# Performance work log

Measured on AMD Instinct MI355X. Metric: run time of the kernel, lower is better.

## Reference

```python
import jax, jax.numpy as jnp
import numpy as np

E = 200_000   # edges (messages)
T = 2_000_000 # triplets
N = 20_000    # atoms/nodes
H = 128       # hidden_channels
INT = 64      # int_emb_size
BAS = 8       # basis_emb_size
OUT_EMB = 256 # out_emb_channels
NRAD = 6
SBF_DIM = 7 * 6  # num_spherical * num_radial = 42
NB = 4        # num_blocks
OUTC = 1      # num_targets


def setup_inputs() -> dict:
    key = jax.random.key(0)
    ks = iter(jax.random.split(key, 64))

    def w(shape):
        # glorot-ish scaled weights, stored as [in, out] for x @ W
        return jax.random.normal(next(ks), shape, jnp.float32) / np.sqrt(shape[-2])

    return dict(
        x=jax.random.normal(next(ks), (E, H), jnp.float32),
        rbf=jax.random.normal(next(ks), (E, NRAD), jnp.float32),
        sbf=jax.random.normal(next(ks), (T, SBF_DIM), jnp.float32),
        # interaction block params, stacked over NB blocks
        W_rbf1=w((NB, NRAD, BAS)), W_rbf2=w((NB, BAS, H)),
        W_sbf1=w((NB, SBF_DIM, BAS)), W_sbf2=w((NB, BAS, INT)),
        W_kj=w((NB, H, H)), b_kj=jnp.zeros((NB, H), jnp.float32),
        W_ji=w((NB, H, H)), b_ji=jnp.zeros((NB, H), jnp.float32),
        W_down=w((NB, H, INT)), W_up=w((NB, INT, H)),
        Wb=w((NB, 2, H, H)), bb=jnp.zeros((NB, 2, H), jnp.float32),   # num_before_skip=1 -> 2 linears
        Wa=w((NB, 4, H, H)), ba=jnp.zeros((NB, 4, H), jnp.float32),   # num_after_skip=2 -> 4 linears
        W_lin=w((NB, H, H)), b_lin=jnp.zeros((NB, H), jnp.float32),
        # output block params, stacked over NB+1 blocks
        Wo_rbf=w((NB + 1, NRAD, H)),
        Wo_up=w((NB + 1, H, OUT_EMB)), bo_up=jnp.zeros((NB + 1, OUT_EMB), jnp.float32),
        Wo_lins=w((NB + 1, 3, OUT_EMB, OUT_EMB)), bo_lins=jnp.zeros((NB + 1, 3, OUT_EMB), jnp.float32),
        Wo_out=w((NB + 1, OUT_EMB, OUTC)),
        idx_kj=jax.random.randint(next(ks), (T,), 0, E, jnp.int32),
        idx_ji=jax.random.randint(next(ks), (T,), 0, E, jnp.int32),
        idx_i=jax.random.randint(next(ks), (E,), 0, N, jnp.int32),
        num_nodes=N,
    )


def _interaction(b, x, rbf, sbf, idx_kj, idx_ji, p):
    act = jax.nn.silu
    x_ji = act(x @ p['W_ji'][b] + p['b_ji'][b])
    x_kj = act(x @ p['W_kj'][b] + p['b_kj'][b])
    rbf_t = (rbf @ p['W_rbf1'][b]) @ p['W_rbf2'][b]          # [E,H]
    x_kj = act((x_kj * rbf_t) @ p['W_down'][b])              # [E,INT]
    sbf_t = (sbf @ p['W_sbf1'][b]) @ p['W_sbf2'][b]          # [T,INT]
    m = x_kj[idx_kj] * sbf_t                                  # triplet gather [T,INT]
    agg = jax.ops.segment_sum(m, idx_ji, num_segments=x.shape[0])  # scatter-add [E,INT]
    x_kj = act(agg @ p['W_up'][b])                            # [E,H]
    h = x_ji + x_kj
    # residual layers before skip (1 layer = 2 linears)
    h = h + act(act(h @ p['Wb'][b, 0] + p['bb'][b, 0]) @ p['Wb'][b, 1] + p['bb'][b, 1])
    h = act(h @ p['W_lin'][b] + p['b_lin'][b]) + x
    # residual layers after skip (2 layers = 4 linears)
    for l in range(2):
        h = h + act(act(h @ p['Wa'][b, 2 * l] + p['ba'][b, 2 * l]) @ p['Wa'][b, 2 * l + 1] + p['ba'][b, 2 * l + 1])
    return h


def _output(b, x, rbf, idx_i, num_nodes, p):
    act = jax.nn.silu
    t = (rbf @ p['Wo_rbf'][b]) * x                            # [E,H]
    t = jax.ops.segment_sum(t, idx_i, num_segments=num_nodes) # [N,H]
    t = t @ p['Wo_up'][b] + p['bo_up'][b]
    for l in range(3):
        t = act(t @ p['Wo_lins'][b, l] + p['bo_lins'][b, l])
    return t @ p['Wo_out'][b]                                 # [N,OUTC]


def reference(x, rbf, sbf, W_rbf1, W_rbf2, W_sbf1, W_sbf2, W_kj, b_kj, W_ji, b_ji,
              W_down, W_up, Wb, bb, Wa, ba, W_lin, b_lin,
              Wo_rbf, Wo_up, bo_up, Wo_lins, bo_lins, Wo_out,
              idx_kj, idx_ji, idx_i, num_nodes):
    p = dict(W_rbf1=W_rbf1, W_rbf2=W_rbf2, W_sbf1=W_sbf1, W_sbf2=W_sbf2,
             W_kj=W_kj, b_kj=b_kj, W_ji=W_ji, b_ji=b_ji, W_down=W_down, W_up=W_up,
             Wb=Wb, bb=bb, Wa=Wa, ba=ba, W_lin=W_lin, b_lin=b_lin,
             Wo_rbf=Wo_rbf, Wo_up=Wo_up, bo_up=bo_up,
             Wo_lins=Wo_lins, bo_lins=bo_lins, Wo_out=Wo_out)
    P = _output(0, x, rbf, idx_i, num_nodes, p)
    for b in range(NB):  # fixed small layer loop
        x = _interaction(b, x, rbf, sbf, idx_kj, idx_ji, p)
        P = P + _output(b + 1, x, rbf, idx_i, num_nodes, p)
    return P
```

## Files before the change

kernel.cpp:

```cpp
#include <hip/hip_runtime.h>
#include <hip/hip_bf16.h>

#define E_EDGES 200000
#define T_TRIP  2000000
#define N_NODES 20000
#define H_DIM   128
#define INT_DIM 64
#define BAS     8
#define OUT_EMB 256
#define NRAD    6
#define SBF_D   42
#define NB      4

typedef __attribute__((ext_vector_type(8))) __bf16 bf16x8;
typedef __attribute__((ext_vector_type(4))) float f32x4;
typedef unsigned short u16;

__device__ __forceinline__ float silu_f(float v) { return v / (1.0f + __expf(-v)); }

__device__ __forceinline__ u16 f2bf(float f) {
    unsigned int u = __float_as_uint(f);
    u += 0x7FFF + ((u >> 16) & 1);
    return (u16)(u >> 16);
}
__device__ __forceinline__ float bf2f(u16 h) {
    return __uint_as_float(((unsigned int)h) << 16);
}

__device__ __forceinline__ void st_split4(char* H, char* L, int row, int col0, int stride,
                                          const float v[4]) {
    ushort4 hh, ll;
    u16 h0 = f2bf(v[0]); ll.x = f2bf(v[0] - bf2f(h0)); hh.x = h0;
    u16 h1 = f2bf(v[1]); ll.y = f2bf(v[1] - bf2f(h1)); hh.y = h1;
    u16 h2 = f2bf(v[2]); ll.z = f2bf(v[2] - bf2f(h2)); hh.z = h2;
    u16 h3 = f2bf(v[3]); ll.w = f2bf(v[3] - bf2f(h3)); hh.w = h3;
    int off = (row * stride + col0 * 2) ^ ((row & 7) << 4);
    *reinterpret_cast<ushort4*>(H + off) = hh;
    *reinterpret_cast<ushort4*>(L + off) = ll;
}
__device__ __forceinline__ void ld_split4(const char* H, const char* L, int row, int col0,
                                          int stride, float v[4]) {
    int off = (row * stride + col0 * 2) ^ ((row & 7) << 4);
    ushort4 hh = *reinterpret_cast<const ushort4*>(H + off);
    ushort4 ll = *reinterpret_cast<const ushort4*>(L + off);
    v[0] = bf2f(hh.x) + bf2f(ll.x);
    v[1] = bf2f(hh.y) + bf2f(ll.y);
    v[2] = bf2f(hh.z) + bf2f(ll.z);
    v[3] = bf2f(hh.w) + bf2f(ll.w);
}

struct BF8x4 { bf16x8 h[4]; bf16x8 l[4]; };

__device__ __forceinline__ BF8x4 loadB128f(const u16* __restrict__ Bh, const u16* __restrict__ Bl,
                                           int k0, int wn, int l15, int khalf)
{
    BF8x4 f;
    #pragma unroll
    for (int n = 0; n < 4; ++n) {
        size_t bo = (size_t)(wn * 64 + n * 16 + l15) * 128 + k0 + khalf;
        f.h[n] = *reinterpret_cast<const bf16x8*>(Bh + bo);
        f.l[n] = *reinterpret_cast<const bf16x8*>(Bl + bo);
    }
    return f;
}
__device__ __forceinline__ BF8x4 loadB64f(const u16* __restrict__ Bh, const u16* __restrict__ Bl,
                                          int k0, int wn, int l15, int khalf)
{
    BF8x4 f;
    #pragma unroll
    for (int n = 0; n < 4; ++n) {
        size_t bo = (size_t)(wn * 64 + n * 16 + l15) * 64 + k0 + khalf;
        f.h[n] = *reinterpret_cast<const bf16x8*>(Bh + bo);
        f.l[n] = *reinterpret_cast<const bf16x8*>(Bl + bo);
    }
    return f;
}
__device__ __forceinline__ BF8x4 loadB256f(const u16* __restrict__ Bh, const u16* __restrict__ Bl,
                                           int k0, int wn, int l15, int khalf)
{
    BF8x4 f;
    #pragma unroll
    for (int n = 0; n < 4; ++n) {
        size_t bo = (size_t)(wn * 64 + n * 16 + l15) * 256 + k0 + khalf;
        f.h[n] = *reinterpret_cast<const bf16x8*>(Bh + bo);
        f.l[n] = *reinterpret_cast<const bf16x8*>(Bl + bo);
    }
    return f;
}

__device__ __forceinline__ void mfma_cluster(
    const char* AH, const char* AL, int k0, int wm, int l15, int khalf,
    const BF8x4& b, f32x4 acc[2][4])
{
    __builtin_amdgcn_s_setprio(1);
    #pragma unroll
    for (int m = 0; m < 2; ++m) {
        int row = wm * 32 + m * 16 + l15;
        int off = (row * 256 + (k0 + khalf) * 2) ^ ((row & 7) << 4);
        bf16x8 ah = *reinterpret_cast<const bf16x8*>(AH + off);
        bf16x8 al = *reinterpret_cast<const bf16x8*>(AL + off);
        #pragma unroll
        for (int n = 0; n < 4; ++n) {
            acc[m][n] = __builtin_amdgcn_mfma_f32_16x16x32_bf16(b.h[n], ah, acc[m][n], 0, 0, 0);
            acc[m][n] = __builtin_amdgcn_mfma_f32_16x16x32_bf16(b.h[n], al, acc[m][n], 0, 0, 0);
            acc[m][n] = __builtin_amdgcn_mfma_f32_16x16x32_bf16(b.l[n], ah, acc[m][n], 0, 0, 0);
        }
    }
    __builtin_amdgcn_s_setprio(0);
}
__device__ __forceinline__ void mfma_cluster64(
    const char* AH, const char* AL, int k0, int wm, int l15, int khalf,
    const BF8x4& b, f32x4 acc[2][4])
{
    __builtin_amdgcn_s_setprio(1);
    #pragma unroll
    for (int m = 0; m < 2; ++m) {
        int row = wm * 32 + m * 16 + l15;
        int off = (row * 128 + (k0 + khalf) * 2) ^ ((row & 7) << 4);
        bf16x8 ah = *reinterpret_cast<const bf16x8*>(AH + off);
        bf16x8 al = *reinterpret_cast<const bf16x8*>(AL + off);
        #pragma unroll
        for (int n = 0; n < 4; ++n) {
            acc[m][n] = __builtin_amdgcn_mfma_f32_16x16x32_bf16(b.h[n], ah, acc[m][n], 0, 0, 0);
            acc[m][n] = __builtin_amdgcn_mfma_f32_16x16x32_bf16(b.h[n], al, acc[m][n], 0, 0, 0);
            acc[m][n] = __builtin_amdgcn_mfma_f32_16x16x32_bf16(b.l[n], ah, acc[m][n], 0, 0, 0);
        }
    }
    __builtin_amdgcn_s_setprio(0);
}
__device__ __forceinline__ void mfma_cluster512(
    const char* AH, const char* AL, int k0, int l15, int khalf,
    const BF8x4& b, f32x4 acc[2][4])
{
    __builtin_amdgcn_s_setprio(1);
    #pragma unroll
    for (int m = 0; m < 2; ++m) {
        int row = m * 16 + l15;
        int off = (row * 512 + (k0 + khalf) * 2) ^ ((row & 7) << 4);
        bf16x8 ah = *reinterpret_cast<const bf16x8*>(AH + off);
        bf16x8 al = *reinterpret_cast<const bf16x8*>(AL + off);
        #pragma unroll
        for (int n = 0; n < 4; ++n) {
            acc[m][n] = __builtin_amdgcn_mfma_f32_16x16x32_bf16(b.h[n], ah, acc[m][n], 0, 0, 0);
            acc[m][n] = __builtin_amdgcn_mfma_f32_16x16x32_bf16(b.h[n], al, acc[m][n], 0, 0, 0);
            acc[m][n] = __builtin_amdgcn_mfma_f32_16x16x32_bf16(b.l[n], ah, acc[m][n], 0, 0, 0);
        }
    }
    __builtin_amdgcn_s_setprio(0);
}

__device__ __forceinline__ void mm128_pipe(
    const char* AH, const char* AL,
    const u16* __restrict__ Bh, const u16* __restrict__ Bl, BF8x4& pre,
    const u16* __restrict__ nBh, const u16* __restrict__ nBl,
    int wm, int wn, int l15, int khalf, f32x4 acc[2][4])
{
    BF8x4 c0 = pre;
    BF8x4 c1 = loadB128f(Bh, Bl, 32, wn, l15, khalf);
    mfma_cluster(AH, AL, 0, wm, l15, khalf, c0, acc);
    BF8x4 c2 = loadB128f(Bh, Bl, 64, wn, l15, khalf);
    mfma_cluster(AH, AL, 32, wm, l15, khalf, c1, acc);
    BF8x4 c3 = loadB128f(Bh, Bl, 96, wn, l15, khalf);
    mfma_cluster(AH, AL, 64, wm, l15, khalf, c2, acc);
    if (nBh) pre = loadB128f(nBh, nBl, 0, wn, l15, khalf);
    mfma_cluster(AH, AL, 96, wm, l15, khalf, c3, acc);
}
__device__ __forceinline__ void mm64_pipe(
    const char* AH, const char* AL,
    const u16* __restrict__ Bh, const u16* __restrict__ Bl, BF8x4& pre,
    const u16* __restrict__ nBh, const u16* __restrict__ nBl,
    int wm, int wn, int l15, int khalf, f32x4 acc[2][4])
{
    BF8x4 c0 = pre;
    BF8x4 c1 = loadB64f(Bh, Bl, 32, wn, l15, khalf);
    mfma_cluster64(AH, AL, 0, wm, l15, khalf, c0, acc);
    if (nBh) pre = loadB128f(nBh, nBl, 0, wn, l15, khalf);
    mfma_cluster64(AH, AL, 32, wm, l15, khalf, c1, acc);
}

__global__ __launch_bounds__(256) void wprep(
    const float* __restrict__ src, u16* __restrict__ hi,
    u16* __restrict__ lo, int K, int N)
{
    int e = blockIdx.x * 256 + threadIdx.x;
    int total = K * N;
    if (e >= total) return;
    size_t base = (size_t)blockIdx.y * total;
    float a = src[base + e];
    int k = e / N, n = e - k * N;
    u16 h = f2bf(a);
    u16 l = f2bf(a - bf2f(h));
    hi[base + (size_t)n * K + k] = h;
    lo[base + (size_t)n * K + k] = l;
}

__global__ __launch_bounds__(256, 2) void pre_fuse(
    const float* __restrict__ X, const float* __restrict__ rbf,
    const float* __restrict__ W1,
    const u16* __restrict__ Wjih, const u16* __restrict__ Wjil, const float* __restrict__ bji,
    const u16* __restrict__ Wkjh, const u16* __restrict__ Wkjl, const float* __restrict__ bkj,
    const float* __restrict__ Wr2,
    const u16* __restrict__ Wdnh, const u16* __restrict__ Wdnl,
    float* __restrict__ E1, float* __restrict__ C1)
{
    __shared__ u16 XH[64 * 128], XL[64 * 128];
    __shared__ u16 IH[64 * 128], IL[64 * 128];

    const int tid  = threadIdx.x;
    const int lane = tid & 63;
    const int w    = tid >> 6;
    const int wm   = w >> 1, wn = w & 1;
    const int bm   = blockIdx.x * 64;
    const int l15  = lane & 15;
    const int khalf = (lane >> 4) * 8;
    const int r4   = (lane >> 4) * 4;

    BF8x4 pre = loadB128f(Wjih, Wjil, 0, wn, l15, khalf);

    {
        int r  = tid >> 2;
        int c0 = (tid & 3) * 32;
        const float* p = &X[(size_t)(bm + r) * H_DIM + c0];
        const int swz = (r & 7) << 4;
        #pragma unroll
        for (int q = 0; q < 8; ++q) {
            float4 f = *reinterpret_cast<const float4*>(p + q * 4);
            float vv[4] = {f.x, f.y, f.z, f.w};
            u16 h[4], l[4];
            #pragma unroll
            for (int j = 0; j < 4; ++j) {
                h[j] = f2bf(vv[j]);
                l[j] = f2bf(vv[j] - bf2f(h[j]));
            }
            int off = (r * 256 + c0 * 2 + q * 8) ^ swz;
            *reinterpret_cast<ushort4*>((char*)XH + off) = make_ushort4(h[0], h[1], h[2], h[3]);
            *reinterpret_cast<ushort4*>((char*)XL + off) = make_ushort4(l[0], l[1], l[2], l[3]);
        }
    }
    __syncthreads();

    {
        f32x4 acc[2][4] = {};
        mm128_pipe((char*)XH, (char*)XL, Wjih, Wjil, pre, Wkjh, Wkjl,
                   wm, wn, l15, khalf, acc);
        #pragma unroll
        for (int n = 0; n < 4; ++n) {
            int col0 = wn * 64 + n * 16 + r4;
            float4 bv = *reinterpret_cast<const float4*>(&bji[col0]);
            #pragma unroll
            for (int m = 0; m < 2; ++m) {
                int row = wm * 32 + m * 16 + l15;
                float4 o;
                o.x = silu_f(acc[m][n][0] + bv.x);
                o.y = silu_f(acc[m][n][1] + bv.y);
                o.z = silu_f(acc[m][n][2] + bv.z);
                o.w = silu_f(acc[m][n][3] + bv.w);
                *reinterpret_cast<float4*>(&E1[(size_t)(bm + row) * H_DIM + col0]) = o;
            }
        }
    }
    {
        f32x4 acc[2][4] = {};
        mm128_pipe((char*)XH, (char*)XL, Wkjh, Wkjl, pre, nullptr, nullptr,
                   wm, wn, l15, khalf, acc);
        float r8v[2][8];
        #pragma unroll
        for (int m = 0; m < 2; ++m) {
            int grow = bm + wm * 32 + m * 16 + l15;
            const float2* rp = reinterpret_cast<const float2*>(&rbf[(size_t)grow * NRAD]);
            float2 q0 = rp[0], q1 = rp[1], q2 = rp[2];
            float rv[NRAD] = {q0.x, q0.y, q1.x, q1.y, q2.x, q2.y};
            #pragma unroll
            for (int j = 0; j < 8; ++j) r8v[m][j] = 0.f;
            #pragma unroll
            for (int k = 0; k < NRAD; ++k)
                #pragma unroll
                for (int j = 0; j < 8; ++j)
                    r8v[m][j] = fmaf(rv[k], W1[k * BAS + j], r8v[m][j]);
        }
        #pragma unroll
        for (int n = 0; n < 4; ++n) {
            int col0 = wn * 64 + n * 16 + r4;
            float4 bvf = *reinterpret_cast<const float4*>(&bkj[col0]);
            float bv[4] = {bvf.x, bvf.y, bvf.z, bvf.w};
            float wrv[8][4];
            #pragma unroll
            for (int j = 0; j < 8; ++j) {
                float4 wf = *reinterpret_cast<const float4*>(&Wr2[j * H_DIM + col0]);
                wrv[j][0] = wf.x; wrv[j][1] = wf.y; wrv[j][2] = wf.z; wrv[j][3] = wf.w;
            }
            #pragma unroll
            for (int m = 0; m < 2; ++m) {
                int row = wm * 32 + m * 16 + l15;
                float v[4];
                #pragma unroll
                for (int r = 0; r < 4; ++r) {
                    float t = silu_f(acc[m][n][r] + bv[r]);
                    float g = 0.f;
                    #pragma unroll
                    for (int j = 0; j < 8; ++j)
                        g = fmaf(r8v[m][j], wrv[j][r], g);
                    v[r] = t * g;
                }
                st_split4((char*)IH, (char*)IL, row, col0, 256, v);
            }
        }
    }
    __syncthreads();

    {
        f32x4 acc[2][2] = {};
        #pragma unroll
        for (int k0 = 0; k0 < 128; k0 += 32) {
            bf16x8 bh[2], bl[2];
            #pragma unroll
            for (int n = 0; n < 2; ++n) {
                size_t bo = (size_t)(wn * 32 + n * 16 + l15) * 128 + k0 + khalf;
                bh[n] = *reinterpret_cast<const bf16x8*>(Wdnh + bo);
                bl[n] = *reinterpret_cast<const bf16x8*>(Wdnl + bo);
            }
            __builtin_amdgcn_s_setprio(1);
            #pragma unroll
            for (int m = 0; m < 2; ++m) {
                int row = wm * 32 + m * 16 + l15;
                int off = (row * 256 + (k0 + khalf) * 2) ^ ((row & 7) << 4);
                bf16x8 ah = *reinterpret_cast<const bf16x8*>((const char*)IH + off);
                bf16x8 al = *reinterpret_cast<const bf16x8*>((const char*)IL + off);
                #pragma unroll
                for (int n = 0; n < 2; ++n) {
                    acc[m][n] = __builtin_amdgcn_mfma_f32_16x16x32_bf16(bh[n], ah, acc[m][n], 0, 0, 0);
                    acc[m][n] = __builtin_amdgcn_mfma_f32_16x16x32_bf16(bh[n], al, acc[m][n], 0, 0, 0);
                    acc[m][n] = __builtin_amdgcn_mfma_f32_16x16x32_bf16(bl[n], ah, acc[m][n], 0, 0, 0);
                }
            }
            __builtin_amdgcn_s_setprio(0);
        }
        #pragma unroll
        for (int n = 0; n < 2; ++n) {
            int col0 = wn * 32 + n * 16 + r4;
            #pragma unroll
            for (int m = 0; m < 2; ++m) {
                int row = wm * 32 + m * 16 + l15;
                float4 o;
                o.x = silu_f(acc[m][n][0]);
                o.y = silu_f(acc[m][n][1]);
                o.z = silu_f(acc[m][n][2]);
                o.w = silu_f(acc[m][n][3]);
                *reinterpret_cast<float4*>(&C1[(size_t)(bm + row) * INT_DIM + col0]) = o;
            }
        }
    }
}

struct ChainP {
    const u16 *uph, *upl;
    const u16 *b0h, *b0l, *b1h, *b1l;
    const u16 *lnh, *lnl;
    const u16 *a0h, *a0l, *a1h, *a1l, *a2h, *a2l, *a3h, *a3l;
    const float *bb0, *bb1, *blin, *ba0, *ba1, *ba2, *ba3;
};
struct OutP {
    const float* TN;
    const u16 *Uh, *Ul; const float* bu;
    const u16 *L0h, *L0l; const float* b0;
    const u16 *L1h, *L1l; const float* b1;
    const u16 *L2h, *L2l; const float* b2;
    const float* Wo; float* P;
};

__device__ __forceinline__ void post_chain_body(
    char* smem, int bx,
    const float* __restrict__ AGG, const float* __restrict__ E1,
    const float* __restrict__ X, const ChainP& p, float* __restrict__ OUT)
{
    char* GH  = smem;
    char* GL  = smem + 8192;
    char* P0H = smem + 16384;
    char* P0L = smem + 32768;
    char* P1H = smem + 49152;
    char* P1L = smem + 65536;

    const int tid  = threadIdx.x;
    const int lane = tid & 63;
    const int w    = tid >> 6;
    const int wm   = w >> 1, wn = w & 1;
    const int bm   = bx * 64;
    const int l15  = lane & 15;
    const int khalf = (lane >> 4) * 8;
    const int r4   = (lane >> 4) * 4;

    BF8x4 pre = loadB64f(p.uph, p.upl, 0, wn, l15, khalf);

    {
        int r  = tid >> 2;
        int c0 = (tid & 3) * 16;
        const float* pg = &AGG[(size_t)(bm + r) * INT_DIM + c0];
        const int swz = (r & 7) << 4;
        #pragma unroll
        for (int q = 0; q < 4; ++q) {
            float4 f = *reinterpret_cast<const float4*>(pg + q * 4);
            float vv[4] = {f.x, f.y, f.z, f.w};
            u16 h[4], l[4];
            #pragma unroll
            for (int j = 0; j < 4; ++j) {
                h[j] = f2bf(vv[j]);
                l[j] = f2bf(vv[j] - bf2f(h[j]));
            }
            int off = (r * 128 + c0 * 2 + q * 8) ^ swz;
            *reinterpret_cast<ushort4*>(GH + off) = make_ushort4(h[0], h[1], h[2], h[3]);
            *reinterpret_cast<ushort4*>(GL + off) = make_ushort4(l[0], l[1], l[2], l[3]);
        }
    }
    __syncthreads();

    f32x4 acc[2][4];

    #pragma unroll
    for (int m = 0; m < 2; ++m)
        #pragma unroll
        for (int n = 0; n < 4; ++n) acc[m][n] = f32x4{0.f, 0.f, 0.f, 0.f};
    mm64_pipe(GH, GL, p.uph, p.upl, pre, p.b0h, p.b0l, wm, wn, l15, khalf, acc);
    #pragma unroll
    for (int n = 0; n < 4; ++n) {
        int col0 = wn * 64 + n * 16 + r4;
        #pragma unroll
        for (int m = 0; m < 2; ++m) {
            int row = wm * 32 + m * 16 + l15;
            float4 e = *reinterpret_cast<const float4*>(&E1[(size_t)(bm + row) * H_DIM + col0]);
            float v[4];
            v[0] = e.x + silu_f(acc[m][n][0]);
            v[1] = e.y + silu_f(acc[m][n][1]);
            v[2] = e.z + silu_f(acc[m][n][2]);
            v[3] = e.w + silu_f(acc[m][n][3]);
            st_split4(P0H, P0L, row, col0, 256, v);
        }
    }
    __syncthreads();

    #define STAGE_PLAIN(SRC_H, SRC_L, WH, WL, BIAS, DST_H, DST_L, NWH, NWL)             \
    {                                                                                   \
        _Pragma("unroll")                                                               \
        for (int m = 0; m < 2; ++m)                                                     \
            _Pragma("unroll")                                                           \
            for (int n = 0; n < 4; ++n) acc[m][n] = f32x4{0.f, 0.f, 0.f, 0.f};          \
        mm128_pipe(SRC_H, SRC_L, WH, WL, pre, NWH, NWL, wm, wn, l15, khalf, acc);       \
        _Pragma("unroll")                                                               \
        for (int n = 0; n < 4; ++n) {                                                   \
            int col0 = wn * 64 + n * 16 + r4;                                           \
            float4 bv = *reinterpret_cast<const float4*>(&BIAS[col0]);                  \
            _Pragma("unroll")                                                           \
            for (int m = 0; m < 2; ++m) {                                               \
                int row = wm * 32 + m * 16 + l15;                                       \
                float v[4];                                                             \
                v[0] = silu_f(acc[m][n][0] + bv.x);                                     \
                v[1] = silu_f(acc[m][n][1] + bv.y);                                     \
                v[2] = silu_f(acc[m][n][2] + bv.z);                                     \
                v[3] = silu_f(acc[m][n][3] + bv.w);                                     \
                st_split4(DST_H, DST_L, row, col0, 256, v);                             \
            }                                                                           \
        }                                                                               \
        __syncthreads();                                                                \
    }

    #define STAGE_RES(SRC_H, SRC_L, WH, WL, BIAS, RES_H, RES_L, NWH, NWL)               \
    {                                                                                   \
        _Pragma("unroll")                                                               \
        for (int m = 0; m < 2; ++m)                                                     \
            _Pragma("unroll")                                                           \
            for (int n = 0; n < 4; ++n) acc[m][n] = f32x4{0.f, 0.f, 0.f, 0.f};          \
        mm128_pipe(SRC_H, SRC_L, WH, WL, pre, NWH, NWL, wm, wn, l15, khalf, acc);       \
        _Pragma("unroll")                                                               \
        for (int n = 0; n < 4; ++n) {                                                   \
            int col0 = wn * 64 + n * 16 + r4;                                           \
            float4 bv = *reinterpret_cast<const float4*>(&BIAS[col0]);                  \
            _Pragma("unroll")                                                           \
            for (int m = 0; m < 2; ++m) {                                               \
                int row = wm * 32 + m * 16 + l15;                                       \
                float v[4];                                                             \
                ld_split4(RES_H, RES_L, row, col0, 256, v);                             \
                v[0] += silu_f(acc[m][n][0] + bv.x);                                    \
                v[1] += silu_f(acc[m][n][1] + bv.y);                                    \
                v[2] += silu_f(acc[m][n][2] + bv.z);                                    \
                v[3] += silu_f(acc[m][n][3] + bv.w);                                    \
                st_split4(RES_H, RES_L, row, col0, 256, v);                             \
            }                                                                           \
        }                                                                               \
        __syncthreads();                                                                \
    }

    STAGE_PLAIN(P0H, P0L, p.b0h, p.b0l, p.bb0, P1H, P1L, p.b1h, p.b1l)
    STAGE_RES(P1H, P1L, p.b1h, p.b1l, p.bb1, P0H, P0L, p.lnh, p.lnl)

    {
        #pragma unroll
        for (int m = 0; m < 2; ++m)
            #pragma unroll
            for (int n = 0; n < 4; ++n) acc[m][n] = f32x4{0.f, 0.f, 0.f, 0.f};
        mm128_pipe(P0H, P0L, p.lnh, p.lnl, pre, p.a0h, p.a0l, wm, wn, l15, khalf, acc);
        #pragma unroll
        for (int n = 0; n < 4; ++n) {
            int col0 = wn * 64 + n * 16 + r4;
            float4 bv = *reinterpret_cast<const float4*>(&p.blin[col0]);
            #pragma unroll
            for (int m = 0; m < 2; ++m) {
                int row = wm * 32 + m * 16 + l15;
                float4 xv = *reinterpret_cast<const float4*>(&X[(size_t)(bm + row) * H_DIM + col0]);
                float v[4];
                v[0] = silu_f(acc[m][n][0] + bv.x) + xv.x;
                v[1] = silu_f(acc[m][n][1] + bv.y) + xv.y;
                v[2] = silu_f(acc[m][n][2] + bv.z) + xv.z;
                v[3] = silu_f(acc[m][n][3] + bv.w) + xv.w;
                st_split4(P1H, P1L, row, col0, 256, v);
            }
        }
        __syncthreads();
    }

    STAGE_PLAIN(P1H, P1L, p.a0h, p.a0l, p.ba0, P0H, P0L, p.a1h, p.a1l)
    STAGE_RES(P0H, P0L, p.a1h, p.a1l, p.ba1, P1H, P1L, p.a2h, p.a2l)
    STAGE_PLAIN(P1H, P1L, p.a2h, p.a2l, p.ba2, P0H, P0L, p.a3h, p.a3l)

    {
        #pragma unroll
        for (int m = 0; m < 2; ++m)
            #pragma unroll
            for (int n = 0; n < 4; ++n) acc[m][n] = f32x4{0.f, 0.f, 0.f, 0.f};
        mm128_pipe(P0H, P0L, p.a3h, p.a3l, pre, nullptr, nullptr, wm, wn, l15, khalf, acc);
        #pragma unroll
        for (int n = 0; n < 4; ++n) {
            int col0 = wn * 64 + n * 16 + r4;
            float4 bv = *reinterpret_cast<const float4*>(&p.ba3[col0]);
            #pragma unroll
            for (int m = 0; m < 2; ++m) {
                int row = wm * 32 + m * 16 + l15;
                float v[4];
                ld_split4(P1H, P1L, row, col0, 256, v);
                float4 o;
                o.x = v[0] + silu_f(acc[m][n][0] + bv.x);
                o.y = v[1] + silu_f(acc[m][n][1] + bv.y);
                o.z = v[2] + silu_f(acc[m][n][2] + bv.z);
                o.w = v[3] + silu_f(acc[m][n][3] + bv.w);
                *reinterpret_cast<float4*>(&OUT[(size_t)(bm + row) * H_DIM + col0]) = o;
            }
        }
    }
    #undef STAGE_PLAIN
    #undef STAGE_RES
}

__device__ __forceinline__ void out_chain_body(char* smem, int bx, const OutP& o)
{
    char* XH  = smem;
    char* XL  = smem + 8192;
    char* T0H = smem + 16384;
    char* T0L = smem + 32768;
    char* T1H = smem + 49152;
    char* T1L = smem + 65536;

    const int tid  = threadIdx.x;
    const int lane = tid & 63;
    const int wn   = tid >> 6;
    const int bm   = bx * 32;
    const int l15  = lane & 15;
    const int khalf = (lane >> 4) * 8;
    const int r4   = (lane >> 4) * 4;

    {
        int r  = tid >> 3;
        int c0 = (tid & 7) * 16;
        const float* p = &o.TN[(size_t)(bm + r) * H_DIM + c0];
        const int swz = (r & 7) << 4;
        #pragma unroll
        for (int q = 0; q < 4; ++q) {
            float4 f = *reinterpret_cast<const float4*>(p + q * 4);
            float vv[4] = {f.x, f.y, f.z, f.w};
            u16 h[4], l[4];
            #pragma unroll
            for (int j = 0; j < 4; ++j) {
                h[j] = f2bf(vv[j]);
                l[j] = f2bf(vv[j] - bf2f(h[j]));
            }
            int off = (r * 256 + c0 * 2 + q * 8) ^ swz;
            *reinterpret_cast<ushort4*>(XH + off) = make_ushort4(h[0], h[1], h[2], h[3]);
            *reinterpret_cast<ushort4*>(XL + off) = make_ushort4(l[0], l[1], l[2], l[3]);
        }
    }
    __syncthreads();

    f32x4 acc[2][4];

    {
        #pragma unroll
        for (int m = 0; m < 2; ++m)
            #pragma unroll
            for (int n = 0; n < 4; ++n) acc[m][n] = f32x4{0.f, 0.f, 0.f, 0.f};
        BF8x4 cur = loadB128f(o.Uh, o.Ul, 0, wn, l15, khalf);
        #pragma unroll
        for (int k = 0; k < 4; ++k) {
            BF8x4 nxt;
            if (k < 3) nxt = loadB128f(o.Uh, o.Ul, 32 * (k + 1), wn, l15, khalf);
            mfma_cluster(XH, XL, 32 * k, 0, l15, khalf, cur, acc);
            if (k < 3) cur = nxt;
        }
        #pragma unroll
        for (int n = 0; n < 4; ++n) {
            int col0 = wn * 64 + n * 16 + r4;
            float4 bv = *reinterpret_cast<const float4*>(&o.bu[col0]);
            #pragma unroll
            for (int m = 0; m < 2; ++m) {
                int row = m * 16 + l15;
                float v[4] = {acc[m][n][0] + bv.x, acc[m][n][1] + bv.y,
                              acc[m][n][2] + bv.z, acc[m][n][3] + bv.w};
                st_split4(T0H, T0L, row, col0, 512, v);
            }
        }
        __syncthreads();
    }

    #define OLIN(SRC_H, SRC_L, WH, WL, BIAS, DST_H, DST_L)                              \
    {                                                                                   \
        _Pragma("unroll")                                                               \
        for (int m = 0; m < 2; ++m)                                                     \
            _Pragma("unroll")                                                           \
            for (int n = 0; n < 4; ++n) acc[m][n] = f32x4{0.f, 0.f, 0.f, 0.f};          \
        BF8x4 cur = loadB256f(WH, WL, 0, wn, l15, khalf);                               \
        _Pragma("unroll")                                                               \
        for (int k = 0; k < 8; ++k) {                                                   \
            BF8x4 nxt;                                                                  \
            if (k < 7) nxt = loadB256f(WH, WL, 32 * (k + 1), wn, l15, khalf);           \
            mfma_cluster512(SRC_H, SRC_L, 32 * k, l15, khalf, cur, acc);                \
            if (k < 7) cur = nxt;                                                       \
        }                                                                               \
        _Pragma("unroll")                                                               \
        for (int n = 0; n < 4; ++n) {                                                   \
            int col0 = wn * 64 + n * 16 + r4;                                           \
            float4 bv = *reinterpret_cast<const float4*>(&BIAS[col0]);                  \
            _Pragma("unroll")                                                           \
            for (int m = 0; m < 2; ++m) {                                               \
                int row = m * 16 + l15;                                                 \
                float v[4];                                                             \
                v[0] = silu_f(acc[m][n][0] + bv.x);                                     \
                v[1] = silu_f(acc[m][n][1] + bv.y);                                     \
                v[2] = silu_f(acc[m][n][2] + bv.z);                                     \
                v[3] = silu_f(acc[m][n][3] + bv.w);                                     \
                st_split4(DST_H, DST_L, row, col0, 512, v);                             \
            }                                                                           \
        }                                                                               \
        __syncthreads();                                                                \
    }

    OLIN(T0H, T0L, o.L0h, o.L0l, o.b0, T1H, T1L)
    OLIN(T1H, T1L, o.L1h, o.L1l, o.b1, T0H, T0L)
    OLIN(T0H, T0L, o.L2h, o.L2l, o.b2, T1H, T1L)
    #undef OLIN

    {
        int row  = tid >> 3;
        int part = tid & 7;
        float s = 0.f;
        int cbase = part * 32;
        #pragma unroll
        for (int c4 = 0; c4 < 32; c4 += 4) {
            float v[4];
            ld_split4(T1H, T1L, row, cbase + c4, 512, v);
            float4 wv = *reinterpret_cast<const float4*>(&o.Wo[cbase + c4]);
            s = fmaf(v[0], wv.x, s);
            s = fmaf(v[1], wv.y, s);
            s = fmaf(v[2], wv.z, s);
            s = fmaf(v[3], wv.w, s);
        }
        s += __shfl_xor(s, 1);
        s += __shfl_xor(s, 2);
        s += __shfl_xor(s, 4);
        if (part == 0) o.P[bm + row] += s;
    }
}

__global__ __launch_bounds__(256, 2) void post_fused(
    int npost,
    const float* __restrict__ AGG, const float* __restrict__ E1,
    const float* __restrict__ X, ChainP p, float* __restrict__ OUT, OutP o)
{
    __shared__ char smem[81920];
    if ((int)blockIdx.x < npost)
        post_chain_body(smem, blockIdx.x, AGG, E1, X, p, OUT);
    else
        out_chain_body(smem, blockIdx.x - npost, o);
}

__device__ __forceinline__ float dot8_bf(uint4 r, const float* w2) {
    float s;
    s  = bf2f((u16)(r.x)) * w2[0] + bf2f((u16)(r.x >> 16)) * w2[1];
    s += bf2f((u16)(r.y)) * w2[2] + bf2f((u16)(r.y >> 16)) * w2[3];
    s += bf2f((u16)(r.z)) * w2[4] + bf2f((u16)(r.z >> 16)) * w2[5];
    s += bf2f((u16)(r.w)) * w2[6] + bf2f((u16)(r.w >> 16)) * w2[7];
    return s;
}

__device__ __forceinline__ void triplet_body(
    int bx, int nblk,
    const u16* __restrict__ ps8b, const float* __restrict__ Wsb2,
    const float* __restrict__ xkj, const int* __restrict__ pkj,
    const int* __restrict__ tptr, const int* __restrict__ tcnt,
    float* __restrict__ agg)
{
    const int lane = threadIdx.x & 63;
    int wid = bx * 4 + (threadIdx.x >> 6);
    const int nw = nblk * 4;
    float w2[BAS];
    #pragma unroll
    for (int j = 0; j < BAS; ++j) w2[j] = Wsb2[j * INT_DIM + lane];

    for (int e = wid; e < E_EDGES; e += nw) {
        int start = tptr[e];
        int end   = start + tcnt[e];
        float acc0 = 0.f, acc1 = 0.f;
        int i = start;
        for (; i + 1 < end; i += 2) {
            uint4 ra = *reinterpret_cast<const uint4*>(&ps8b[(size_t)i * BAS]);
            uint4 rb = *reinterpret_cast<const uint4*>(&ps8b[(size_t)(i + 1) * BAS]);
            int e0 = pkj[i], e1 = pkj[i + 1];
            float s0 = dot8_bf(ra, w2);
            float s1 = dot8_bf(rb, w2);
            acc0 = fmaf(xkj[(size_t)e0 * INT_DIM + lane], s0, acc0);
            acc1 = fmaf(xkj[(size_t)e1 * INT_DIM + lane], s1, acc1);
        }
        if (i < end) {
            uint4 ra = *reinterpret_cast<const uint4*>(&ps8b[(size_t)i * BAS]);
            int e0 = pkj[i];
            acc0 = fmaf(xkj[(size_t)e0 * INT_DIM + lane], dot8_bf(ra, w2), acc0);
        }
        agg[(size_t)e * INT_DIM + lane] = acc0 + acc1;
    }
}

__device__ __forceinline__ void out_gather_body(
    int bx, int nblk,
    const float* __restrict__ rbf, const float* __restrict__ Wor,
    const float* __restrict__ x,
    const int* __restrict__ eptr, const int* __restrict__ ecnt,
    const int* __restrict__ eperm, float* __restrict__ tN)
{
    const int lane = threadIdx.x & 63;
    int wid = bx * 4 + (threadIdx.x >> 6);
    const int nw = nblk * 4;
    float wr0[NRAD], wr1[NRAD];
    #pragma unroll
    for (int k = 0; k < NRAD; ++k) {
        wr0[k] = Wor[k * H_DIM + lane];
        wr1[k] = Wor[k * H_DIM + lane + 64];
    }
    for (int n = wid; n < N_NODES; n += nw) {
        int start = eptr[n];
        int end   = start + ecnt[n];
        float a0 = 0.f, a1 = 0.f;
        for (int i = start; i < end; ++i) {
            int e = eperm[i];
            const float2* rp = reinterpret_cast<const float2*>(&rbf[(size_t)e * NRAD]);
            float2 r0 = rp[0], r1 = rp[1], r2 = rp[2];
            float rA = r0.x*wr0[0] + r0.y*wr0[1] + r1.x*wr0[2]
                     + r1.y*wr0[3] + r2.x*wr0[4] + r2.y*wr0[5];
            float rB = r0.x*wr1[0] + r0.y*wr1[1] + r1.x*wr1[2]
                     + r1.y*wr1[3] + r2.x*wr1[4] + r2.y*wr1[5];
            a0 = fmaf(rA, x[(size_t)e * H_DIM + lane], a0);
            a1 = fmaf(rB, x[(size_t)e * H_DIM + lane + 64], a1);
        }
        tN[(size_t)n * H_DIM + lane] = a0;
        tN[(size_t)n * H_DIM + lane + 64] = a1;
    }
}

__global__ __launch_bounds__(256) void gather_fused(
    int GT,
    const u16* __restrict__ ps8b, const float* __restrict__ Wsb2,
    const float* __restrict__ xkj, const int* __restrict__ pkj,
    const int* __restrict__ tptr, const int* __restrict__ tcnt,
    float* __restrict__ agg,
    const float* __restrict__ rbf, const float* __restrict__ Wor,
    const float* __restrict__ x,
    const int* __restrict__ eptr, const int* __restrict__ ecnt,
    const int* __restrict__ eperm, float* __restrict__ tN)
{
    int bx = blockIdx.x;
    if (bx < GT)
        triplet_body(bx, GT, ps8b, Wsb2, xkj, pkj, tptr, tcnt, agg);
    else
        out_gather_body(bx - GT, gridDim.x - GT, rbf, Wor, x, eptr, ecnt, eperm, tN);
}

__global__ __launch_bounds__(256) void csr_count(
    const int* __restrict__ idx, int* __restrict__ cnt, int n)
{
    int i = blockIdx.x * 256 + threadIdx.x;
    if (i < n) atomicAdd(&cnt[idx[i]], 1);
}

__global__ __launch_bounds__(256) void scan_block(
    const int* __restrict__ cnt, int* __restrict__ ptr, int* __restrict__ bsum, int n)
{
    __shared__ int s[256];
    int i = blockIdx.x * 256 + threadIdx.x;
    int v = (i < n) ? cnt[i] : 0;
    s[threadIdx.x] = v;
    __syncthreads();
    #pragma unroll
    for (int off = 1; off < 256; off <<= 1) {
        int t = (threadIdx.x >= off) ? s[threadIdx.x - off] : 0;
        __syncthreads();
        s[threadIdx.x] += t;
        __syncthreads();
    }
    if (i < n) ptr[i] = s[threadIdx.x] - v;
    if (threadIdx.x == 255) bsum[blockIdx.x] = s[255];
}

__global__ __launch_bounds__(1024) void scan_aux(int* __restrict__ bsum, int nb)
{
    __shared__ int s[1024];
    int v = (threadIdx.x < nb) ? bsum[threadIdx.x] : 0;
    s[threadIdx.x] = v;
    __syncthreads();
    #pragma unroll
    for (int off = 1; off < 1024; off <<= 1) {
        int t = (threadIdx.x >= off) ? s[threadIdx.x - off] : 0;
        __syncthreads();
        s[threadIdx.x] += t;
        __syncthreads();
    }
    if (threadIdx.x < nb) bsum[threadIdx.x] = s[threadIdx.x] - v;
}

__global__ __launch_bounds__(256) void scan_add(
    int* __restrict__ ptr, const int* __restrict__ bsum, int n)
{
    int i = blockIdx.x * 256 + threadIdx.x;
    if (i < n) ptr[i] += bsum[blockIdx.x];
// ... 232 lines not shown
```

Before: 4.168 ms.

## Store intermediate activations as single bf16 to cut LDS and raise occupancy

Activations that feed only the next GEMM are now kept in LDS as one bf16 value instead of a hi/lo split pair. Their matmuls drop the lo-activation MFMA term (two MFMAs instead of three per tile). Buffers are reorganised into one split residual stream plus one bf16 temp, with extra barriers where stages now overwrite in place. Shared memory falls from 80KB to 48KB and launch bounds rise to 3 blocks per CU, aiming at higher occupancy and fewer MFMAs, at the cost of reduced precision on those intermediates.

```diff
diff --git a/kernel.cpp b/kernel.cpp
--- a/kernel.cpp
+++ b/kernel.cpp
@@ -48,6 +48,13 @@
     v[2] = bf2f(hh.z) + bf2f(ll.z);
     v[3] = bf2f(hh.w) + bf2f(ll.w);
 }
+__device__ __forceinline__ void st_bf4(char* T, int row, int col0, int stride,
+                                       const float v[4]) {
+    ushort4 hh;
+    hh.x = f2bf(v[0]); hh.y = f2bf(v[1]); hh.z = f2bf(v[2]); hh.w = f2bf(v[3]);
+    int off = (row * stride + col0 * 2) ^ ((row & 7) << 4);
+    *reinterpret_cast<ushort4*>(T + off) = hh;
+}
 
 struct BF8x4 { bf16x8 h[4]; bf16x8 l[4]; };
 
@@ -108,6 +115,24 @@
     }
     __builtin_amdgcn_s_setprio(0);
 }
+__device__ __forceinline__ void mfma_cluster_T(
+    const char* T, int k0, int wm, int l15, int khalf,
+    const BF8x4& b, f32x4 acc[2][4])
+{
+    __builtin_amdgcn_s_setprio(1);
+    #pragma unroll
+    for (int m = 0; m < 2; ++m) {
+        int row = wm * 32 + m * 16 + l15;
+        int off = (row * 256 + (k0 + khalf) * 2) ^ ((row & 7) << 4);
+        bf16x8 a = *reinterpret_cast<const bf16x8*>(T + off);
+        #pragma unroll
+        for (int n = 0; n < 4; ++n) {
+            acc[m][n] = __builtin_amdgcn_mfma_f32_16x16x32_bf16(b.h[n], a, acc[m][n], 0, 0, 0);
+            acc[m][n] = __builtin_amdgcn_mfma_f32_16x16x32_bf16(b.l[n], a, acc[m][n], 0, 0, 0);
+        }
+    }
+    __builtin_amdgcn_s_setprio(0);
+}
 __device__ __forceinline__ void mfma_cluster64(
     const char* AH, const char* AL, int k0, int wm, int l15, int khalf,
     const BF8x4& b, f32x4 acc[2][4])
@@ -144,6 +169,24 @@
             acc[m][n] = __builtin_amdgcn_mfma_f32_16x16x32_bf16(b.h[n], ah, acc[m][n], 0, 0, 0);
             acc[m][n] = __builtin_amdgcn_mfma_f32_16x16x32_bf16(b.h[n], al, acc[m][n], 0, 0, 0);
             acc[m][n] = __builtin_amdgcn_mfma_f32_16x16x32_bf16(b.l[n], ah, acc[m][n], 0, 0, 0);
+        }
+    }
+    __builtin_amdgcn_s_setprio(0);
+}
+__device__ __forceinline__ void mfma_cluster512_T(
+    const char* T, int k0, int l15, int khalf,
+    const BF8x4& b, f32x4 acc[2][4])
+{
+    __builtin_amdgcn_s_setprio(1);
+    #pragma unroll
+    for (int m = 0; m < 2; ++m) {
+        int row = m * 16 + l15;
+        int off = (row * 512 + (k0 + khalf) * 2) ^ ((row & 7) << 4);
+        bf16x8 a = *reinterpret_cast<const bf16x8*>(T + off);
+        #pragma unroll
+        for (int n = 0; n < 4; ++n) {
+            acc[m][n] = __builtin_amdgcn_mfma_f32_16x16x32_bf16(b.h[n], a, acc[m][n], 0, 0, 0);
+            acc[m][n] = __builtin_amdgcn_mfma_f32_16x16x32_bf16(b.l[n], a, acc[m][n], 0, 0, 0);
         }
     }
     __builtin_amdgcn_s_setprio(0);
@@ -164,6 +207,22 @@
     mfma_cluster(AH, AL, 64, wm, l15, khalf, c2, acc);
     if (nBh) pre = loadB128f(nBh, nBl, 0, wn, l15, khalf);
     mfma_cluster(AH, AL, 96, wm, l15, khalf, c3, acc);
+}
+__device__ __forceinline__ void mm128_pipe_T(
+    const char* T,
+    const u16* __restrict__ Bh, const u16* __restrict__ Bl, BF8x4& pre,
+    const u16* __restrict__ nBh, const u16* __restrict__ nBl,
+    int wm, int wn, int l15, int khalf, f32x4 acc[2][4])
+{
+    BF8x4 c0 = pre;
+    BF8x4 c1 = loadB128f(Bh, Bl, 32, wn, l15, khalf);
+    mfma_cluster_T(T, 0, wm, l15, khalf, c0, acc);
+    BF8x4 c2 = loadB128f(Bh, Bl, 64, wn, l15, khalf);
+    mfma_cluster_T(T, 32, wm, l15, khalf, c1, acc);
+    BF8x4 c3 = loadB128f(Bh, Bl, 96, wn, l15, khalf);
+    mfma_cluster_T(T, 64, wm, l15, khalf, c2, acc);
+    if (nBh) pre = loadB128f(nBh, nBl, 0, wn, l15, khalf);
+    mfma_cluster_T(T, 96, wm, l15, khalf, c3, acc);
 }
 __device__ __forceinline__ void mm64_pipe(
     const char* AH, const char* AL,
@@ -194,7 +253,7 @@
     lo[base + (size_t)n * K + k] = l;
 }
 
-__global__ __launch_bounds__(256, 2) void pre_fuse(
+__global__ __launch_bounds__(256, 3) void pre_fuse(
     const float* __restrict__ X, const float* __restrict__ rbf,
     const float* __restrict__ W1,
     const u16* __restrict__ Wjih, const u16* __restrict__ Wjil, const float* __restrict__ bji,
@@ -203,8 +262,10 @@
     const u16* __restrict__ Wdnh, const u16* __restrict__ Wdnl,
     float* __restrict__ E1, float* __restrict__ C1)
 {
-    __shared__ u16 XH[64 * 128], XL[64 * 128];
-    __shared__ u16 IH[64 * 128], IL[64 * 128];
+    __shared__ char smem[49152];
+    char* XH = smem;
+    char* XL = smem + 16384;
+    char* IT = smem + 32768;
 
     const int tid  = threadIdx.x;
     const int lane = tid & 63;
@@ -233,16 +294,15 @@
                 l[j] = f2bf(vv[j] - bf2f(h[j]));
             }
             int off = (r * 256 + c0 * 2 + q * 8) ^ swz;
-            *reinterpret_cast<ushort4*>((char*)XH + off) = make_ushort4(h[0], h[1], h[2], h[3]);
-            *reinterpret_cast<ushort4*>((char*)XL + off) = make_ushort4(l[0], l[1], l[2], l[3]);
+            *reinterpret_cast<ushort4*>(XH + off) = make_ushort4(h[0], h[1], h[2], h[3]);
+            *reinterpret_cast<ushort4*>(XL + off) = make_ushort4(l[0], l[1], l[2], l[3]);
         }
     }
     __syncthreads();
 
     {
         f32x4 acc[2][4] = {};
-        mm128_pipe((char*)XH, (char*)XL, Wjih, Wjil, pre, Wkjh, Wkjl,
-                   wm, wn, l15, khalf, acc);
+        mm128_pipe(XH, XL, Wjih, Wjil, pre, Wkjh, Wkjl, wm, wn, l15, khalf, acc);
         #pragma unroll
         for (int n = 0; n < 4; ++n) {
             int col0 = wn * 64 + n * 16 + r4;
@@ -261,8 +321,7 @@
     }
     {
         f32x4 acc[2][4] = {};
-        mm128_pipe((char*)XH, (char*)XL, Wkjh, Wkjl, pre, nullptr, nullptr,
-                   wm, wn, l15, khalf, acc);
+        mm128_pipe(XH, XL, Wkjh, Wkjl, pre, nullptr, nullptr, wm, wn, l15, khalf, acc);
         float r8v[2][8];
         #pragma unroll
         for (int m = 0; m < 2; ++m) {
@@ -302,7 +361,7 @@
                         g = fmaf(r8v[m][j], wrv[j][r], g);
                     v[r] = t * g;
                 }
-                st_split4((char*)IH, (char*)IL, row, col0, 256, v);
+                st_bf4(IT, row, col0, 256, v);
             }
         }
     }
@@ -324,13 +383,11 @@
             for (int m = 0; m < 2; ++m) {
                 int row = wm * 32 + m * 16 + l15;
                 int off = (row * 256 + (k0 + khalf) * 2) ^ ((row & 7) << 4);
-                bf16x8 ah = *reinterpret_cast<const bf16x8*>((const char*)IH + off);
-                bf16x8 al = *reinterpret_cast<const bf16x8*>((const char*)IL + off);
+                bf16x8 a = *reinterpret_cast<const bf16x8*>(IT + off);
                 #pragma unroll
                 for (int n = 0; n < 2; ++n) {
-                    acc[m][n] = __builtin_amdgcn_mfma_f32_16x16x32_bf16(bh[n], ah, acc[m][n], 0, 0, 0);
-                    acc[m][n] = __builtin_amdgcn_mfma_f32_16x16x32_bf16(bh[n], al, acc[m][n], 0, 0, 0);
-                    acc[m][n] = __builtin_amdgcn_mfma_f32_16x16x32_bf16(bl[n], ah, acc[m][n], 0, 0, 0);
+                    acc[m][n] = __builtin_amdgcn_mfma_f32_16x16x32_bf16(bh[n], a, acc[m][n], 0, 0, 0);
+                    acc[m][n] = __builtin_amdgcn_mfma_f32_16x16x32_bf16(bl[n], a, acc[m][n], 0, 0, 0);
                 }
             }
             __builtin_amdgcn_s_setprio(0);
@@ -373,12 +430,11 @@
     const float* __restrict__ AGG, const float* __restrict__ E1,
     const float* __restrict__ X, const ChainP& p, float* __restrict__ OUT)
 {
-    char* GH  = smem;
-    char* GL  = smem + 8192;
-    char* P0H = smem + 16384;
-    char* P0L = smem + 32768;
-    char* P1H = smem + 49152;
-    char* P1L = smem + 65536;
+    char* SH  = smem;
+    char* SL  = smem + 16384;
+    char* TMP = smem + 32768;
+    char* GH  = TMP;
+    char* GL  = TMP + 8192;
 
     const int tid  = threadIdx.x;
     const int lane = tid & 63;
@@ -414,11 +470,11 @@
     __syncthreads();
 
     f32x4 acc[2][4];
-
-    #pragma unroll
-    for (int m = 0; m < 2; ++m)
-        #pragma unroll
-        for (int n = 0; n < 4; ++n) acc[m][n] = f32x4{0.f, 0.f, 0.f, 0.f};
+    #define ZACC { _Pragma("unroll") for (int m = 0; m < 2; ++m) \
+                   _Pragma("unroll") for (int n = 0; n < 4; ++n) \
+                       acc[m][n] = f32x4{0.f, 0.f, 0.f, 0.f}; }
+
+    ZACC
     mm64_pipe(GH, GL, p.uph, p.upl, pre, p.b0h, p.b0l, wm, wn, l15, khalf, acc);
     #pragma unroll
     for (int n = 0; n < 4; ++n) {
@@ -432,18 +488,15 @@
             v[1] = e.y + silu_f(acc[m][n][1]);
             v[2] = e.z + silu_f(acc[m][n][2]);
             v[3] = e.w + silu_f(acc[m][n][3]);
-            st_split4(P0H, P0L, row, col0, 256, v);
+            st_split4(SH, SL, row, col0, 256, v);
         }
     }
     __syncthreads();
 
-    #define STAGE_PLAIN(SRC_H, SRC_L, WH, WL, BIAS, DST_H, DST_L, NWH, NWL)             \
+    #define STAGE_PLAIN(WH, WL, BIAS, NWH, NWL)                                         \
     {                                                                                   \
-        _Pragma("unroll")                                                               \
-        for (int m = 0; m < 2; ++m)                                                     \
-            _Pragma("unroll")                                                           \
-            for (int n = 0; n < 4; ++n) acc[m][n] = f32x4{0.f, 0.f, 0.f, 0.f};          \
-        mm128_pipe(SRC_H, SRC_L, WH, WL, pre, NWH, NWL, wm, wn, l15, khalf, acc);       \
+        ZACC                                                                            \
+        mm128_pipe(SH, SL, WH, WL, pre, NWH, NWL, wm, wn, l15, khalf, acc);             \
         _Pragma("unroll")                                                               \
         for (int n = 0; n < 4; ++n) {                                                   \
             int col0 = wn * 64 + n * 16 + r4;                                           \
@@ -456,19 +509,16 @@
                 v[1] = silu_f(acc[m][n][1] + bv.y);                                     \
                 v[2] = silu_f(acc[m][n][2] + bv.z);                                     \
                 v[3] = silu_f(acc[m][n][3] + bv.w);                                     \
-                st_split4(DST_H, DST_L, row, col0, 256, v);                             \
+                st_bf4(TMP, row, col0, 256, v);                                         \
             }                                                                           \
         }                                                                               \
         __syncthreads();                                                                \
     }
 
-    #define STAGE_RES(SRC_H, SRC_L, WH, WL, BIAS, RES_H, RES_L, NWH, NWL)               \
+    #define STAGE_RES(WH, WL, BIAS, NWH, NWL)                                           \
     {                                                                                   \
-        _Pragma("unroll")                                                               \
-        for (int m = 0; m < 2; ++m)                                                     \
-            _Pragma("unroll")                                                           \
-            for (int n = 0; n < 4; ++n) acc[m][n] = f32x4{0.f, 0.f, 0.f, 0.f};          \
-        mm128_pipe(SRC_H, SRC_L, WH, WL, pre, NWH, NWL, wm, wn, l15, khalf, acc);       \
+        ZACC                                                                            \
+        mm128_pipe_T(TMP, WH, WL, pre, NWH, NWL, wm, wn, l15, khalf, acc);              \
         _Pragma("unroll")                                                               \
         for (int n = 0; n < 4; ++n) {                                                   \
             int col0 = wn * 64 + n * 16 + r4;                                           \
@@ -477,26 +527,24 @@
             for (int m = 0; m < 2; ++m) {                                               \
                 int row = wm * 32 + m * 16 + l15;                                       \
                 float v[4];                                                             \
-                ld_split4(RES_H, RES_L, row, col0, 256, v);                             \
+                ld_split4(SH, SL, row, col0, 256, v);                                   \
                 v[0] += silu_f(acc[m][n][0] + bv.x);                                    \
                 v[1] += silu_f(acc[m][n][1] + bv.y);                                    \
                 v[2] += silu_f(acc[m][n][2] + bv.z);                                    \
                 v[3] += silu_f(acc[m][n][3] + bv.w);                                    \
-                st_split4(RES_H, RES_L, row, col0, 256, v);                             \
+                st_split4(SH, SL, row, col0, 256, v);                                   \
             }                                                                           \
         }                                                                               \
         __syncthreads();                                                                \
     }
 
-    STAGE_PLAIN(P0H, P0L, p.b0h, p.b0l, p.bb0, P1H, P1L, p.b1h, p.b1l)
-    STAGE_RES(P1H, P1L, p.b1h, p.b1l, p.bb1, P0H, P0L, p.lnh, p.lnl)
-
-    {
-        #pragma unroll
-        for (int m = 0; m < 2; ++m)
-            #pragma unroll
-            for (int n = 0; n < 4; ++n) acc[m][n] = f32x4{0.f, 0.f, 0.f, 0.f};
-        mm128_pipe(P0H, P0L, p.lnh, p.lnl, pre, p.a0h, p.a0l, wm, wn, l15, khalf, acc);
+    STAGE_PLAIN(p.b0h, p.b0l, p.bb0, p.b1h, p.b1l)
+    STAGE_RES(p.b1h, p.b1l, p.bb1, p.lnh, p.lnl)
+
+    {
+        ZACC
+        mm128_pipe(SH, SL, p.lnh, p.lnl, pre, p.a0h, p.a0l, wm, wn, l15, khalf, acc);
+        __syncthreads();
         #pragma unroll
         for (int n = 0; n < 4; ++n) {
             int col0 = wn * 64 + n * 16 + r4;
@@ -510,22 +558,19 @@
                 v[1] = silu_f(acc[m][n][1] + bv.y) + xv.y;
                 v[2] = silu_f(acc[m][n][2] + bv.z) + xv.z;
                 v[3] = silu_f(acc[m][n][3] + bv.w) + xv.w;
-                st_split4(P1H, P1L, row, col0, 256, v);
+                st_split4(SH, SL, row, col0, 256, v);
             }
         }
         __syncthreads();
     }
 
-    STAGE_PLAIN(P1H, P1L, p.a0h, p.a0l, p.ba0, P0H, P0L, p.a1h, p.a1l)
-    STAGE_RES(P0H, P0L, p.a1h, p.a1l, p.ba1, P1H, P1L, p.a2h, p.a2l)
-    STAGE_PLAIN(P1H, P1L, p.a2h, p.a2l, p.ba2, P0H, P0L, p.a3h, p.a3l)
-
-    {
-        #pragma unroll
-        for (int m = 0; m < 2; ++m)
-            #pragma unroll
-            for (int n = 0; n < 4; ++n) acc[m][n] = f32x4{0.f, 0.f, 0.f, 0.f};
-        mm128_pipe(P0H, P0L, p.a3h, p.a3l, pre, nullptr, nullptr, wm, wn, l15, khalf, acc);
+    STAGE_PLAIN(p.a0h, p.a0l, p.ba0, p.a1h, p.a1l)
+    STAGE_RES(p.a1h, p.a1l, p.ba1, p.a2h, p.a2l)
+    STAGE_PLAIN(p.a2h, p.a2l, p.ba2, p.a3h, p.a3l)
+
+    {
+        ZACC
+        mm128_pipe_T(TMP, p.a3h, p.a3l, pre, nullptr, nullptr, wm, wn, l15, khalf, acc);
         #pragma unroll
         for (int n = 0; n < 4; ++n) {
             int col0 = wn * 64 + n * 16 + r4;
@@ -534,7 +579,7 @@
             for (int m = 0; m < 2; ++m) {
                 int row = wm * 32 + m * 16 + l15;
                 float v[4];
-                ld_split4(P1H, P1L, row, col0, 256, v);
+                ld_split4(SH, SL, row, col0, 256, v);
                 float4 o;
                 o.x = v[0] + silu_f(acc[m][n][0] + bv.x);
                 o.y = v[1] + silu_f(acc[m][n][1] + bv.y);
@@ -546,16 +591,16 @@
     }
     #undef STAGE_PLAIN
     #undef STAGE_RES
+    #undef ZACC
 }
 
 __device__ __forceinline__ void out_chain_body(char* smem, int bx, const OutP& o)
 {
-    char* XH  = smem;
-    char* XL  = smem + 8192;
-    char* T0H = smem + 16384;
-    char* T0L = smem + 32768;
-    char* T1H = smem + 49152;
-    char* T1L = smem + 65536;
+    char* SH  = smem;
+    char* SL  = smem + 16384;
+    char* TMP = smem + 32768;
+    char* XH  = TMP;
+    char* XL  = TMP + 8192;
 
     const int tid  = threadIdx.x;
     const int lane = tid & 63;
@@ -588,12 +633,12 @@
     __syncthreads();
 
     f32x4 acc[2][4];
-
-    {
-        #pragma unroll
-        for (int m = 0; m < 2; ++m)
-            #pragma unroll
-            for (int n = 0; n < 4; ++n) acc[m][n] = f32x4{0.f, 0.f, 0.f, 0.f};
+    #define ZACC { _Pragma("unroll") for (int m = 0; m < 2; ++m) \
+                   _Pragma("unroll") for (int n = 0; n < 4; ++n) \
+                       acc[m][n] = f32x4{0.f, 0.f, 0.f, 0.f}; }
+
+    {
+        ZACC
         BF8x4 cur = loadB128f(o.Uh, o.Ul, 0, wn, l15, khalf);
         #pragma unroll
         for (int k = 0; k < 4; ++k) {
@@ -602,6 +647,7 @@
             mfma_cluster(XH, XL, 32 * k, 0, l15, khalf, cur, acc);
             if (k < 3) cur = nxt;
         }
+        __syncthreads();
         #pragma unroll
         for (int n = 0; n < 4; ++n) {
             int col0 = wn * 64 + n * 16 + r4;
@@ -611,48 +657,96 @@
                 int row = m * 16 + l15;
                 float v[4] = {acc[m][n][0] + bv.x, acc[m][n][1] + bv.y,
                               acc[m][n][2] + bv.z, acc[m][n][3] + bv.w};
-                st_split4(T0H, T0L, row, col0, 512, v);
+                st_split4(SH, SL, row, col0, 512, v);
             }
         }
         __syncthreads();
     }
 
-    #define OLIN(SRC_H, SRC_L, WH, WL, BIAS, DST_H, DST_L)                              \
-    {                                                                                   \
-        _Pragma("unroll")                                                               \
-        for (int m = 0; m < 2; ++m)                                                     \
-            _Pragma("unroll")                                                           \
-            for (int n = 0; n < 4; ++n) acc[m][n] = f32x4{0.f, 0.f, 0.f, 0.f};          \
-        BF8x4 cur = loadB256f(WH, WL, 0, wn, l15, khalf);                               \
-        _Pragma("unroll")                                                               \
-        for (int k = 0; k < 8; ++k) {                                                   \
-            BF8x4 nxt;                                                                  \
-            if (k < 7) nxt = loadB256f(WH, WL, 32 * (k + 1), wn, l15, khalf);           \
-            mfma_cluster512(SRC_H, SRC_L, 32 * k, l15, khalf, cur, acc);                \
-            if (k < 7) cur = nxt;                                                       \
-        }                                                                               \
-        _Pragma("unroll")                                                               \
-        for (int n = 0; n < 4; ++n) {                                                   \
-            int col0 = wn * 64 + n * 16 + r4;                                           \
-            float4 bv = *reinterpret_cast<const float4*>(&BIAS[col0]);                  \
-            _Pragma("unroll")                                                           \
-            for (int m = 0; m < 2; ++m) {                                               \
-                int row = m * 16 + l15;                                                 \
-                float v[4];                                                             \
-                v[0] = silu_f(acc[m][n][0] + bv.x);                                     \
-                v[1] = silu_f(acc[m][n][1] + bv.y);                                     \
-                v[2] = silu_f(acc[m][n][2] + bv.z);                                     \
-                v[3] = silu_f(acc[m][n][3] + bv.w);                                     \
-                st_split4(DST_H, DST_L, row, col0, 512, v);                             \
-            }                                                                           \
-        }                                                                               \
-        __syncthreads();                                                                \
-    }
-
-    OLIN(T0H, T0L, o.L0h, o.L0l, o.b0, T1H, T1L)
-    OLIN(T1H, T1L, o.L1h, o.L1l, o.b1, T0H, T0L)
-    OLIN(T0H, T0L, o.L2h, o.L2l, o.b2, T1H, T1L)
-    #undef OLIN
+    {
+        ZACC
+        BF8x4 cur = loadB256f(o.L0h, o.L0l, 0, wn, l15, khalf);
+        #pragma unroll
+        for (int k = 0; k < 8; ++k) {
+            BF8x4 nxt;
+            if (k < 7) nxt = loadB256f(o.L0h, o.L0l, 32 * (k + 1), wn, l15, khalf);
+            mfma_cluster512(SH, SL, 32 * k, l15, khalf, cur, acc);
+            if (k < 7) cur = nxt;
+        }
+        #pragma unroll
+        for (int n = 0; n < 4; ++n) {
+            int col0 = wn * 64 + n * 16 + r4;
+            float4 bv = *reinterpret_cast<const float4*>(&o.b0[col0]);
+            #pragma unroll
+            for (int m = 0; m < 2; ++m) {
+                int row = m * 16 + l15;
+                float v[4];
+                v[0] = silu_f(acc[m][n][0] + bv.x);
+                v[1] = silu_f(acc[m][n][1] + bv.y);
+                v[2] = silu_f(acc[m][n][2] + bv.z);
+                v[3] = silu_f(acc[m][n][3] + bv.w);
+                st_bf4(TMP, row, col0, 512, v);
+            }
+        }
+        __syncthreads();
+    }
+
+    {
+        ZACC
+        BF8x4 cur = loadB256f(o.L1h, o.L1l, 0, wn, l15, khalf);
+        #pragma unroll
+        for (int k = 0; k < 8; ++k) {
+            BF8x4 nxt;
+            if (k < 7) nxt = loadB256f(o.L1h, o.L1l, 32 * (k + 1), wn, l15, khalf);
+            mfma_cluster512_T(TMP, 32 * k, l15, khalf, cur, acc);
+            if (k < 7) cur = nxt;
+        }
+        #pragma unroll
+        for (int n = 0; n < 4; ++n) {
+            int col0 = wn * 64 + n * 16 + r4;
+            float4 bv = *reinterpret_cast<const float4*>(&o.b1[col0]);
+            #pragma unroll
+            for (int m = 0; m < 2; ++m) {
+                int row = m * 16 + l15;
+                float v[4];
+                v[0] = silu_f(acc[m][n][0] + bv.x);
+                v[1] = silu_f(acc[m][n][1] + bv.y);
+                v[2] = silu_f(acc[m][n][2] + bv.z);
+                v[3] = silu_f(acc[m][n][3] + bv.w);
+                st_split4(SH, SL, row, col0, 512, v);
+            }
+        }
+        __syncthreads();
+    }
+
+    {
+        ZACC
+        BF8x4 cur = loadB256f(o.L2h, o.L2l, 0, wn, l15, khalf);
+        #pragma unroll
+        for (int k = 0; k < 8; ++k) {
+            BF8x4 nxt;
+            if (k < 7) nxt = loadB256f(o.L2h, o.L2l, 32 * (k + 1), wn, l15, khalf);
+            mfma_cluster512(SH, SL, 32 * k, l15, khalf, cur, acc);
+            if (k < 7) cur = nxt;
+        }
+        __syncthreads();
+        #pragma unroll
+        for (int n = 0; n < 4; ++n) {
+            int col0 = wn * 64 + n * 16 + r4;
+            float4 bv = *reinterpret_cast<const float4*>(&o.b2[col0]);
+            #pragma unroll
+            for (int m = 0; m < 2; ++m) {
+                int row = m * 16 + l15;
+                float v[4];
+                v[0] = silu_f(acc[m][n][0] + bv.x);
+                v[1] = silu_f(acc[m][n][1] + bv.y);
+                v[2] = silu_f(acc[m][n][2] + bv.z);
+                v[3] = silu_f(acc[m][n][3] + bv.w);
+                st_split4(SH, SL, row, col0, 512, v);
+            }
+        }
+        __syncthreads();
+    }
 
     {
         int row  = tid >> 3;
@@ -662,7 +756,7 @@
         #pragma unroll
         for (int c4 = 0; c4 < 32; c4 += 4) {
             float v[4];
-            ld_split4(T1H, T1L, row, cbase + c4, 512, v);
+            ld_split4(SH, SL, row, cbase + c4, 512, v);
             float4 wv = *reinterpret_cast<const float4*>(&o.Wo[cbase + c4]);
             s = fmaf(v[0], wv.x, s);
             s = fmaf(v[1], wv.y, s);
@@ -674,14 +768,15 @@
         s += __shfl_xor(s, 4);
         if (part == 0) o.P[bm + row] += s;
     }
-}
-
-__global__ __launch_bounds__(256, 2) void post_fused(
+    #undef ZACC
+}
+
+__global__ __launch_bounds__(256, 3) void post_fused(
     int npost,
     const float* __restrict__ AGG, const float* __restrict__ E1,
     const float* __restrict__ X, ChainP p, float* __restrict__ OUT, OutP o)
 {
-    __shared__ char smem[81920];
+    __shared__ char smem[49152];
     if ((int)blockIdx.x < npost)
         post_chain_body(smem, blockIdx.x, AGG, E1, X, p, OUT);
     else
```

Measured after the change: 4.371 ms. 4.9% more time.
